# Kernel optimization log

Hardware: AMD Instinct MI355X
Metric: run time of the kernel (lower is better)

## Reference

```python
import jax, jax.numpy as jnp
import numpy as np

N_NODES = 50000


def _sage_conv(x, src, dst, Wl, Wr, b):
    """SAGEConv with mean aggregation: lin_l(mean_j x_j) + lin_r(x_i) + b."""
    msgs = x[src]                                                # [E, Din] gather
    agg = jax.ops.segment_sum(msgs, dst, num_segments=N_NODES)  # [N, Din] scatter-add
    cnt = jax.ops.segment_sum(jnp.ones((src.shape[0], 1), x.dtype), dst,
                              num_segments=N_NODES)             # [N, 1]
    agg = agg / jnp.maximum(cnt, 1.0)                           # mean
    return agg @ Wl.T + x @ Wr.T + b                            # [N, Dout]


def setup_inputs() -> dict:
    key = jax.random.key(0)
    ks = jax.random.split(key, 8)
    d_in, d_h = 64, 128
    x = jax.random.normal(ks[0], (N_NODES, d_in), dtype=jnp.float32)
    edge_index = jax.random.randint(ks[1], (2, 800000), 0, N_NODES, dtype=jnp.int32)
    s1 = 1.0 / np.sqrt(d_in)
    s2 = 1.0 / np.sqrt(d_h)
    return {
        "x": x,
        "edge_index": edge_index,
        "Wl1": jax.random.normal(ks[2], (d_h, d_in), dtype=jnp.float32) * s1,
        "Wr1": jax.random.normal(ks[3], (d_h, d_in), dtype=jnp.float32) * s1,
        "b1": jnp.zeros((d_h,), dtype=jnp.float32),
        "Wl2": jax.random.normal(ks[4], (d_h, d_h), dtype=jnp.float32) * s2,
        "Wr2": jax.random.normal(ks[5], (d_h, d_h), dtype=jnp.float32) * s2,
        "b2": jnp.zeros((d_h,), dtype=jnp.float32),
    }


def reference(x, edge_index, Wl1, Wr1, b1, Wl2, Wr2, b2):
    src, dst = edge_index[0], edge_index[1]
    # layer 1: conv -> dropout(eval: identity) -> ReLU
    h = jax.nn.relu(_sage_conv(x, src, dst, Wl1, Wr1, b1))
    # layer 2
    h = jax.nn.relu(_sage_conv(h, src, dst, Wl2, Wr2, b2))
    return h
```

## Files before the change

kernel.cpp:

```cpp
#include <hip/hip_runtime.h>

#define N_NODES 50000
#define NBUCK 782
#define BCAP 2048
#define BSHIFT 11

typedef __attribute__((ext_vector_type(8))) short short8;
typedef __attribute__((ext_vector_type(4))) float floatx4;
typedef __attribute__((ext_vector_type(2))) float floatx2;
typedef __attribute__((ext_vector_type(2))) int intx2;

static __device__ __forceinline__ unsigned short f2bf(float f) {
  unsigned int u = __builtin_bit_cast(unsigned int, f);
  u += 0x7fff + ((u >> 16) & 1);
  return (unsigned short)(u >> 16);
}
static __device__ __forceinline__ float bf2f(unsigned short s) {
  unsigned int u = ((unsigned int)s) << 16;
  return __builtin_bit_cast(float, u);
}
static __device__ __forceinline__ void fp8x8_acc(intx2 v, floatx2* ac) {
  ac[0] += __builtin_amdgcn_cvt_pk_f32_fp8(v[0], false);
  ac[1] += __builtin_amdgcn_cvt_pk_f32_fp8(v[0], true);
  ac[2] += __builtin_amdgcn_cvt_pk_f32_fp8(v[1], false);
  ac[3] += __builtin_amdgcn_cvt_pk_f32_fp8(v[1], true);
}


__global__ void __launch_bounds__(512) prep_scatter(
    const float* __restrict__ x,
    const float* __restrict__ Wl1, const float* __restrict__ Wr1,
    const float* __restrict__ Wl2, const float* __restrict__ Wr2,
    unsigned short* __restrict__ xb, unsigned char* __restrict__ xq,
    unsigned short* __restrict__ W1, unsigned short* __restrict__ W2,
    const int* __restrict__ src, const int* __restrict__ dst,
    int* __restrict__ bucket_cur, int* __restrict__ buf, int E, int n) {
  const int t = threadIdx.x;
  const int gid = blockIdx.x * 512 + t;
  const int gsz = gridDim.x * 512;
  for (int i = gid; i < n * 16; i += gsz) {
    float4 v = ((const float4*)x)[i];
    unsigned int lo = (unsigned int)f2bf(v.x) | ((unsigned int)f2bf(v.y) << 16);
    unsigned int hi = (unsigned int)f2bf(v.z) | ((unsigned int)f2bf(v.w) << 16);
    ((uint2*)xb)[i] = make_uint2(lo, hi);
    int q = __builtin_amdgcn_cvt_pk_fp8_f32(v.x, v.y, 0, false);
    q = __builtin_amdgcn_cvt_pk_fp8_f32(v.z, v.w, q, true);
    ((int*)xq)[i] = q;
  }
  for (int i = gid; i < 128 * 128; i += gsz) {
    int c = i >> 7, k = i & 127;
    W1[i] = f2bf(k < 64 ? Wl1[c * 64 + k] : Wr1[c * 64 + k - 64]);
  }
  for (int i = gid; i < 128 * 256; i += gsz) {
    int c = i >> 8, k = i & 255;
    W2[i] = f2bf(k < 128 ? Wl2[c * 128 + k] : Wr2[c * 128 + k - 128]);
  }

  __shared__ int hist[NBUCK];
  __shared__ int base_s[NBUCK];
  for (int i = t; i < NBUCK; i += 512) hist[i] = 0;
  __syncthreads();
  int e0 = blockIdx.x * 2048;
  int sv[4], dv[4], bv[4];
#pragma unroll
  for (int p = 0; p < 4; ++p) {
    int e = e0 + p * 512 + t;
    if (e < E) {
      sv[p] = src[e];
      dv[p] = dst[e];
      bv[p] = dv[p] >> 6;
      atomicAdd(&hist[bv[p]], 1);
    } else bv[p] = -1;
  }
  __syncthreads();
  for (int i = t; i < NBUCK; i += 512) {
    int c = hist[i];
    base_s[i] = c > 0 ? atomicAdd(&bucket_cur[i], c) : 0;
  }
  __syncthreads();
  for (int i = t; i < NBUCK; i += 512) hist[i] = 0;
  __syncthreads();
#pragma unroll
  for (int p = 0; p < 4; ++p) {
    if (bv[p] >= 0) {
      int sub = base_s[bv[p]] + atomicAdd(&hist[bv[p]], 1);
      if (sub < BCAP) buf[(bv[p] << BSHIFT) + sub] = (sv[p] << 6) | (dv[p] & 63);
    }
  }
}


__global__ void __launch_bounds__(512, 6) csr_agg_gemm1(
    int* __restrict__ buf, const int* __restrict__ bucket_cur,
    int* __restrict__ row_start, int* __restrict__ row_cnt,
    const unsigned short* __restrict__ xb, const unsigned char* __restrict__ xq,
    const unsigned short* __restrict__ W1, const float* __restrict__ b1,
    unsigned short* __restrict__ h1, unsigned char* __restrict__ h1q, int n) {
  __shared__ int eb[BCAP];
  __shared__ int gsrc[BCAP];
  __shared__ __align__(16) unsigned short aggS[64 * 72];
  __shared__ int cnt[64];
  __shared__ int tmp[64];
  __shared__ int cur[64];
  const int t = threadIdx.x;
  const int b = blockIdx.x;
  const int node0 = b << 6;
  const int len = min(bucket_cur[b], BCAP);
  int* reg = buf + (b << BSHIFT);

  if (t < 64) cnt[t] = 0;
  __syncthreads();
  for (int i = t; i < len; i += 512) {
    int p = reg[i];
    eb[i] = p;
    atomicAdd(&cnt[p & 63], 1);
  }
  __syncthreads();
  if (t < 64) tmp[t] = cnt[t];
  __syncthreads();
#pragma unroll
  for (int off = 1; off < 64; off <<= 1) {
    int u = (t >= off && t < 64) ? tmp[t - off] : 0;
    __syncthreads();
    if (t < 64) tmp[t] += u;
    __syncthreads();
  }
  if (t < 64) {
    int ex = tmp[t] - cnt[t];
    cur[t] = ex;
    int nd = node0 + t;
    if (nd < n) {
      row_start[nd] = (b << BSHIFT) + ex;
      row_cnt[nd] = cnt[t];
    }
  }
  __syncthreads();
  for (int i = t; i < len; i += 512) {
    int p = eb[i];
    int sub = atomicAdd(&cur[p & 63], 1);
    int s = p >> 6;
    gsrc[sub] = s;
    reg[sub] = s;
  }
  __syncthreads();

  const int lane = t & 63;
  const int wv = t >> 6;
  const int eq = lane >> 3;
  const int cl = lane & 7;
  for (int loc = wv; loc < 64; loc += 8) {
    int nd = node0 + loc;
    int cn = (nd < n) ? cnt[loc] : 0;
    int base = tmp[loc] - cnt[loc];
    floatx2 ac[4], ac2[4];
#pragma unroll
    for (int j = 0; j < 4; ++j) { ac[j] = (floatx2){0.f, 0.f}; ac2[j] = (floatx2){0.f, 0.f}; }
    int e = 0;
    for (; e + 16 <= cn; e += 16) {
      int s0 = gsrc[base + e + eq];
      int s1 = gsrc[base + e + 8 + eq];
      intx2 v0 = *(const intx2*)(xq + (size_t)s0 * 64 + cl * 8);
      intx2 v1 = *(const intx2*)(xq + (size_t)s1 * 64 + cl * 8);
      fp8x8_acc(v0, ac);
      fp8x8_acc(v1, ac2);
    }
    for (; e < cn; e += 8) {
      if (e + eq < cn) {
        int s = gsrc[base + e + eq];
        intx2 v = *(const intx2*)(xq + (size_t)s * 64 + cl * 8);
        fp8x8_acc(v, ac);
      }
    }
    float r[8];
#pragma unroll
    for (int j = 0; j < 4; ++j) {
      floatx2 s2 = ac[j] + ac2[j];
      r[2 * j] = s2[0];
      r[2 * j + 1] = s2[1];
    }
#pragma unroll
    for (int j = 0; j < 8; ++j) {
      r[j] += __shfl_xor(r[j], 8, 64);
      r[j] += __shfl_xor(r[j], 16, 64);
      r[j] += __shfl_xor(r[j], 32, 64);
    }
    if (eq == 0) {
      float inv = 1.0f / (float)max(cn, 1);
      short8 o;
#pragma unroll
      for (int j = 0; j < 8; ++j) o[j] = (short)f2bf(r[j] * inv);
      *(short8*)(aggS + loc * 72 + cl * 8) = o;
    }
  }
  __syncthreads();

  const int m = lane & 15;
  const int q = lane >> 4;
  const int rw = (wv & 1) * 32;
  const int cw = (wv >> 1) * 32;
  floatx4 acc[2][2];
#pragma unroll
  for (int rt = 0; rt < 2; ++rt)
#pragma unroll
    for (int ct = 0; ct < 2; ++ct) acc[rt][ct] = (floatx4){0.f, 0.f, 0.f, 0.f};

  int ra = node0 + rw + m;      if (ra > n - 1) ra = n - 1;
  int rb = node0 + rw + 16 + m; if (rb > n - 1) rb = n - 1;
  const unsigned short* selfA0 = xb + (size_t)ra * 64 + q * 8;
  const unsigned short* selfA1 = xb + (size_t)rb * 64 + q * 8;
  const unsigned short* aggL0 = aggS + (rw + m) * 72 + q * 8;
  const unsigned short* aggL1 = aggS + (rw + 16 + m) * 72 + q * 8;
  const unsigned short* Wc0 = W1 + (size_t)(cw + m) * 128 + q * 8;
  const unsigned short* Wc1 = W1 + (size_t)(cw + 16 + m) * 128 + q * 8;

#pragma unroll
  for (int kc = 0; kc < 2; ++kc) {
    short8 a0 = *(const short8*)(aggL0 + kc * 32);
    short8 a1 = *(const short8*)(aggL1 + kc * 32);
    short8 w0 = *(const short8*)(Wc0 + kc * 32);
    short8 w1 = *(const short8*)(Wc1 + kc * 32);
    acc[0][0] = __builtin_amdgcn_mfma_f32_16x16x32_bf16(a0, w0, acc[0][0], 0, 0, 0);
    acc[0][1] = __builtin_amdgcn_mfma_f32_16x16x32_bf16(a0, w1, acc[0][1], 0, 0, 0);
    acc[1][0] = __builtin_amdgcn_mfma_f32_16x16x32_bf16(a1, w0, acc[1][0], 0, 0, 0);
    acc[1][1] = __builtin_amdgcn_mfma_f32_16x16x32_bf16(a1, w1, acc[1][1], 0, 0, 0);
  }
#pragma unroll
  for (int kc = 0; kc < 2; ++kc) {
    short8 a0 = *(const short8*)(selfA0 + kc * 32);
    short8 a1 = *(const short8*)(selfA1 + kc * 32);
    short8 w0 = *(const short8*)(Wc0 + 64 + kc * 32);
    short8 w1 = *(const short8*)(Wc1 + 64 + kc * 32);
    acc[0][0] = __builtin_amdgcn_mfma_f32_16x16x32_bf16(a0, w0, acc[0][0], 0, 0, 0);
    acc[0][1] = __builtin_amdgcn_mfma_f32_16x16x32_bf16(a0, w1, acc[0][1], 0, 0, 0);
    acc[1][0] = __builtin_amdgcn_mfma_f32_16x16x32_bf16(a1, w0, acc[1][0], 0, 0, 0);
    acc[1][1] = __builtin_amdgcn_mfma_f32_16x16x32_bf16(a1, w1, acc[1][1], 0, 0, 0);
  }

  float bv0 = b1[cw + m], bv1 = b1[cw + 16 + m];
#pragma unroll
  for (int rt = 0; rt < 2; ++rt) {
#pragma unroll
    for (int j = 0; j < 4; ++j) {
      int row = node0 + rw + rt * 16 + q * 4 + j;
      if (row < n) {
        float v0 = acc[rt][0][j] + bv0; v0 = v0 > 0.f ? v0 : 0.f;
        float v1 = acc[rt][1][j] + bv1; v1 = v1 > 0.f ? v1 : 0.f;
        h1[(size_t)row * 128 + cw + m] = f2bf(v0);
        h1[(size_t)row * 128 + cw + 16 + m] = f2bf(v1);
        h1q[(size_t)row * 128 + cw + m] =
            (unsigned char)__builtin_amdgcn_cvt_pk_fp8_f32(v0, v0, 0, false);
        h1q[(size_t)row * 128 + cw + 16 + m] =
            (unsigned char)__builtin_amdgcn_cvt_pk_fp8_f32(v1, v1, 0, false);
      }
    }
  }
}


__global__ void __launch_bounds__(512, 6) agg_gemm2(
    const unsigned short* __restrict__ h1, const unsigned char* __restrict__ h1q,
    const int* __restrict__ row_start, const int* __restrict__ row_cnt,
    const int* __restrict__ buf, const unsigned short* __restrict__ W2,
    const float* __restrict__ b2, float* __restrict__ out, int n) {
  __shared__ int gsrcS[BCAP];
  __shared__ __align__(16) unsigned short aggS[64 * 136];
  const int t = threadIdx.x;
  const int lane = t & 63;
  const int wv = t >> 6;
  const int node0 = blockIdx.x << 6;

  {
    const int4* b4 = (const int4*)(buf + ((size_t)blockIdx.x << BSHIFT));
    ((int4*)gsrcS)[t] = b4[t];
  }
  __syncthreads();

  const int eq = lane >> 4;
  const int cl = lane & 15;
#pragma unroll 1
  for (int lp = 0; lp < 4; ++lp) {
    int locA = wv + lp * 16;
    int locB = locA + 8;
    int ndA = node0 + locA, ndB = node0 + locB;
    int cnA = 0, stA = 0, cnB = 0, stB = 0;
    if (ndA < n) { cnA = row_cnt[ndA]; stA = row_start[ndA] - (blockIdx.x << BSHIFT); }
    if (ndB < n) { cnB = row_cnt[ndB]; stB = row_start[ndB] - (blockIdx.x << BSHIFT); }
    floatx2 aA[4], aA2[4], aB[4], aB2[4];
#pragma unroll
    for (int j = 0; j < 4; ++j) {
      aA[j] = (floatx2){0.f, 0.f}; aA2[j] = (floatx2){0.f, 0.f};
      aB[j] = (floatx2){0.f, 0.f}; aB2[j] = (floatx2){0.f, 0.f};
    }
    int mx = max(cnA, cnB);
    for (int e = 0; e < mx; e += 8) {
      if (e + eq < cnA) {
        int s = gsrcS[stA + e + eq];
        intx2 v = *(const intx2*)(h1q + (size_t)s * 128 + cl * 8);
        fp8x8_acc(v, aA);
      }
      if (e + 4 + eq < cnA) {
        int s = gsrcS[stA + e + 4 + eq];
        intx2 v = *(const intx2*)(h1q + (size_t)s * 128 + cl * 8);
        fp8x8_acc(v, aA2);
      }
      if (e + eq < cnB) {
        int s = gsrcS[stB + e + eq];
        intx2 v = *(const intx2*)(h1q + (size_t)s * 128 + cl * 8);
        fp8x8_acc(v, aB);
      }
      if (e + 4 + eq < cnB) {
        int s = gsrcS[stB + e + 4 + eq];
        intx2 v = *(const intx2*)(h1q + (size_t)s * 128 + cl * 8);
        fp8x8_acc(v, aB2);
      }
    }
    float rA[8], rB[8];
#pragma unroll
    for (int j = 0; j < 4; ++j) {
      floatx2 sA = aA[j] + aA2[j];
      rA[2 * j] = sA[0]; rA[2 * j + 1] = sA[1];
      floatx2 sB = aB[j] + aB2[j];
      rB[2 * j] = sB[0]; rB[2 * j + 1] = sB[1];
    }
#pragma unroll
    for (int j = 0; j < 8; ++j) {
      rA[j] += __shfl_xor(rA[j], 16, 64);
      rA[j] += __shfl_xor(rA[j], 32, 64);
      rB[j] += __shfl_xor(rB[j], 16, 64);
      rB[j] += __shfl_xor(rB[j], 32, 64);
    }
    if (eq == 0) {
      float invA = 1.0f / (float)max(cnA, 1);
      float invB = 1.0f / (float)max(cnB, 1);
      short8 oA, oB;
#pragma unroll
      for (int j = 0; j < 8; ++j) { oA[j] = (short)f2bf(rA[j] * invA); oB[j] = (short)f2bf(rB[j] * invB); }
      *(short8*)(aggS + locA * 136 + cl * 8) = oA;
      *(short8*)(aggS + locB * 136 + cl * 8) = oB;
    }
  }
  __syncthreads();

  const int m = lane & 15;
  const int q = lane >> 4;
  const int rw = (wv & 1) * 32;
  const int cw = (wv >> 1) * 32;
  floatx4 acc[2][2];
#pragma unroll
  for (int rt = 0; rt < 2; ++rt)
#pragma unroll
    for (int ct = 0; ct < 2; ++ct) acc[rt][ct] = (floatx4){0.f, 0.f, 0.f, 0.f};

  int ra = node0 + rw + m;      if (ra > n - 1) ra = n - 1;
  int rb = node0 + rw + 16 + m; if (rb > n - 1) rb = n - 1;
  const unsigned short* selfA0 = h1 + (size_t)ra * 128 + q * 8;
  const unsigned short* selfA1 = h1 + (size_t)rb * 128 + q * 8;
  const unsigned short* aggL0 = aggS + (rw + m) * 136 + q * 8;
  const unsigned short* aggL1 = aggS + (rw + 16 + m) * 136 + q * 8;
  const unsigned short* Wc0 = W2 + (size_t)(cw + m) * 256 + q * 8;
  const unsigned short* Wc1 = W2 + (size_t)(cw + 16 + m) * 256 + q * 8;

#pragma unroll
  for (int kc = 0; kc < 4; ++kc) {
    short8 a0 = *(const short8*)(aggL0 + kc * 32);
    short8 a1 = *(const short8*)(aggL1 + kc * 32);
    short8 w0 = *(const short8*)(Wc0 + kc * 32);
    short8 w1 = *(const short8*)(Wc1 + kc * 32);
    acc[0][0] = __builtin_amdgcn_mfma_f32_16x16x32_bf16(a0, w0, acc[0][0], 0, 0, 0);
    acc[0][1] = __builtin_amdgcn_mfma_f32_16x16x32_bf16(a0, w1, acc[0][1], 0, 0, 0);
    acc[1][0] = __builtin_amdgcn_mfma_f32_16x16x32_bf16(a1, w0, acc[1][0], 0, 0, 0);
    acc[1][1] = __builtin_amdgcn_mfma_f32_16x16x32_bf16(a1, w1, acc[1][1], 0, 0, 0);
  }
#pragma unroll
  for (int kc = 0; kc < 4; ++kc) {
    short8 a0 = *(const short8*)(selfA0 + kc * 32);
    short8 a1 = *(const short8*)(selfA1 + kc * 32);
    short8 w0 = *(const short8*)(Wc0 + 128 + kc * 32);
    short8 w1 = *(const short8*)(Wc1 + 128 + kc * 32);
    acc[0][0] = __builtin_amdgcn_mfma_f32_16x16x32_bf16(a0, w0, acc[0][0], 0, 0, 0);
    acc[0][1] = __builtin_amdgcn_mfma_f32_16x16x32_bf16(a0, w1, acc[0][1], 0, 0, 0);
    acc[1][0] = __builtin_amdgcn_mfma_f32_16x16x32_bf16(a1, w0, acc[1][0], 0, 0, 0);
    acc[1][1] = __builtin_amdgcn_mfma_f32_16x16x32_bf16(a1, w1, acc[1][1], 0, 0, 0);
  }

  float bv0 = b2[cw + m], bv1 = b2[cw + 16 + m];
#pragma unroll
  for (int rt = 0; rt < 2; ++rt) {
#pragma unroll
    for (int j = 0; j < 4; ++j) {
      int row = node0 + rw + rt * 16 + q * 4 + j;
      if (row < n) {
        float v0 = acc[rt][0][j] + bv0; v0 = v0 > 0.f ? v0 : 0.f;
        float v1 = acc[rt][1][j] + bv1; v1 = v1 > 0.f ? v1 : 0.f;
        out[(size_t)row * 128 + cw + m] = v0;
        out[(size_t)row * 128 + cw + 16 + m] = v1;
      }
    }
  }
}


extern "C" void kernel_launch(void* const* d_in, const int* in_sizes, int n_in,
                              void* d_out, int out_size, void* d_ws, size_t ws_size,
                              hipStream_t stream) {
  const int N = N_NODES;
  const int E = in_sizes[1] / 2;
  const float* x   = (const float*)d_in[0];
  const int*   src = (const int*)d_in[1];
  const int*   dst = src + E;
  const float* Wl1 = (const float*)d_in[2];
  const float* Wr1 = (const float*)d_in[3];
  const float* b1  = (const float*)d_in[4];
  const float* Wl2 = (const float*)d_in[5];
  const float* Wr2 = (const float*)d_in[6];
  const float* b2  = (const float*)d_in[7];
  float* out = (float*)d_out;

  unsigned short* xb = (unsigned short*)d_ws;
  unsigned short* h1 = xb + (size_t)N * 64;
  unsigned short* W1 = h1 + (size_t)N * 128;
  unsigned short* W2 = W1 + 128 * 128;
  int* row_start  = (int*)(W2 + 128 * 256);
  int* row_cnt    = row_start + N;
  int* bucket_cur = row_cnt + N;
  int* buf        = bucket_cur + 784;
  unsigned char* xq  = (unsigned char*)(buf + (size_t)NBUCK * BCAP);
  unsigned char* h1q = xq + (size_t)N * 64;

  hipMemsetAsync(bucket_cur, 0, NBUCK * sizeof(int), stream);
  int sb = (E + 2047) / 2048;
  prep_scatter<<<sb, 512, 0, stream>>>(x, Wl1, Wr1, Wl2, Wr2, xb, xq, W1, W2,
                                       src, dst, bucket_cur, buf, E, N);
  csr_agg_gemm1<<<NBUCK, 512, 0, stream>>>(buf, bucket_cur, row_start, row_cnt,
                                           xb, xq, W1, b1, h1, h1q, N);
  agg_gemm2<<<NBUCK, 512, 0, stream>>>(h1, h1q, row_start, row_cnt, buf, W2, b2, out, N);
}
```

Measured before the change: 190.0 us.

## Pad CSR rows to multiples of 8 with zero sentinel node and software-pipeline gathers

```diff
diff --git a/kernel.cpp b/kernel.cpp
--- a/kernel.cpp
+++ b/kernel.cpp
@@ -14,10 +14,6 @@
   unsigned int u = __builtin_bit_cast(unsigned int, f);
   u += 0x7fff + ((u >> 16) & 1);
   return (unsigned short)(u >> 16);
-}
-static __device__ __forceinline__ float bf2f(unsigned short s) {
-  unsigned int u = ((unsigned int)s) << 16;
-  return __builtin_bit_cast(float, u);
 }
 static __device__ __forceinline__ void fp8x8_acc(intx2 v, floatx2* ac) {
   ac[0] += __builtin_amdgcn_cvt_pk_f32_fp8(v[0], false);
@@ -47,6 +43,11 @@
     q = __builtin_amdgcn_cvt_pk_fp8_f32(v.z, v.w, q, true);
     ((int*)xq)[i] = q;
   }
+  {
+    unsigned char* h1q = xq + ((size_t)n + 1) * 64;
+    if (gid < 16) ((int*)(xq + (size_t)n * 64))[gid] = 0;
+    if (gid >= 16 && gid < 48) ((int*)(h1q + (size_t)n * 128))[gid - 16] = 0;
+  }
   for (int i = gid; i < 128 * 128; i += gsz) {
     int c = i >> 7, k = i & 127;
     W1[i] = f2bf(k < 64 ? Wl1[c * 64 + k] : Wr1[c * 64 + k - 64]);
@@ -60,10 +61,10 @@
   __shared__ int base_s[NBUCK];
   for (int i = t; i < NBUCK; i += 512) hist[i] = 0;
   __syncthreads();
-  int e0 = blockIdx.x * 2048;
-  int sv[4], dv[4], bv[4];
-#pragma unroll
-  for (int p = 0; p < 4; ++p) {
+  int e0 = blockIdx.x * 4096;
+  int sv[8], dv[8], bv[8];
+#pragma unroll
+  for (int p = 0; p < 8; ++p) {
     int e = e0 + p * 512 + t;
     if (e < E) {
       sv[p] = src[e];
@@ -81,7 +82,7 @@
   for (int i = t; i < NBUCK; i += 512) hist[i] = 0;
   __syncthreads();
 #pragma unroll
-  for (int p = 0; p < 4; ++p) {
+  for (int p = 0; p < 8; ++p) {
     if (bv[p] >= 0) {
       int sub = base_s[bv[p]] + atomicAdd(&hist[bv[p]], 1);
       if (sub < BCAP) buf[(bv[p] << BSHIFT) + sub] = (sv[p] << 6) | (dv[p] & 63);
@@ -116,7 +117,7 @@
     atomicAdd(&cnt[p & 63], 1);
   }
   __syncthreads();
-  if (t < 64) tmp[t] = cnt[t];
+  if (t < 64) tmp[t] = (cnt[t] + 7) & ~7;
   __syncthreads();
 #pragma unroll
   for (int off = 1; off < 64; off <<= 1) {
@@ -126,7 +127,8 @@
     __syncthreads();
   }
   if (t < 64) {
-    int ex = tmp[t] - cnt[t];
+    int c8 = (cnt[t] + 7) & ~7;
+    int ex = tmp[t] - c8;
     cur[t] = ex;
     int nd = node0 + t;
     if (nd < n) {
@@ -139,8 +141,14 @@
     int p = eb[i];
     int sub = atomicAdd(&cur[p & 63], 1);
     int s = p >> 6;
-    gsrc[sub] = s;
-    reg[sub] = s;
+    if (sub < BCAP) { gsrc[sub] = s; reg[sub] = s; }
+  }
+  __syncthreads();
+  if (t < 64) {
+    int c8 = (cnt[t] + 7) & ~7;
+    int e1 = tmp[t];
+    for (int j = e1 - c8 + cnt[t]; j < e1; ++j)
+      if (j < BCAP) { gsrc[j] = n; reg[j] = n; }
   }
   __syncthreads();
 
@@ -148,48 +156,56 @@
   const int wv = t >> 6;
   const int eq = lane >> 3;
   const int cl = lane & 7;
-  for (int loc = wv; loc < 64; loc += 8) {
-    int nd = node0 + loc;
-    int cn = (nd < n) ? cnt[loc] : 0;
-    int base = tmp[loc] - cnt[loc];
-    floatx2 ac[4], ac2[4];
-#pragma unroll
-    for (int j = 0; j < 4; ++j) { ac[j] = (floatx2){0.f, 0.f}; ac2[j] = (floatx2){0.f, 0.f}; }
-    int e = 0;
-    for (; e + 16 <= cn; e += 16) {
-      int s0 = gsrc[base + e + eq];
-      int s1 = gsrc[base + e + 8 + eq];
-      intx2 v0 = *(const intx2*)(xq + (size_t)s0 * 64 + cl * 8);
-      intx2 v1 = *(const intx2*)(xq + (size_t)s1 * 64 + cl * 8);
-      fp8x8_acc(v0, ac);
-      fp8x8_acc(v1, ac2);
-    }
-    for (; e < cn; e += 8) {
-      if (e + eq < cn) {
-        int s = gsrc[base + e + eq];
-        intx2 v = *(const intx2*)(xq + (size_t)s * 64 + cl * 8);
-        fp8x8_acc(v, ac);
-      }
-    }
-    float r[8];
+#pragma unroll 1
+  for (int p = 0; p < 4; ++p) {
+    int locA = wv + p * 16;
+    int locB = locA + 8;
+    int cnA = cnt[locA], cnB = cnt[locB];
+    int cpA = (cnA + 7) & ~7, cpB = (cnB + 7) & ~7;
+    int baseA = tmp[locA] - cpA;
+    int baseB = tmp[locB] - cpB;
+    floatx2 aA[4], aB[4];
+#pragma unroll
+    for (int j = 0; j < 4; ++j) { aA[j] = (floatx2){0.f, 0.f}; aB[j] = (floatx2){0.f, 0.f}; }
+    int mx = max(cpA, cpB);
+    int sA = (0 < cpA) ? gsrc[baseA + eq] : n;
+    int sB = (0 < cpB) ? gsrc[baseB + eq] : n;
+    intx2 vA = *(const intx2*)(xq + (size_t)sA * 64 + cl * 8);
+    intx2 vB = *(const intx2*)(xq + (size_t)sB * 64 + cl * 8);
+    for (int e = 8; e < mx; e += 8) {
+      int sA1 = (e < cpA) ? gsrc[baseA + e + eq] : n;
+      int sB1 = (e < cpB) ? gsrc[baseB + e + eq] : n;
+      intx2 vA1 = *(const intx2*)(xq + (size_t)sA1 * 64 + cl * 8);
+      intx2 vB1 = *(const intx2*)(xq + (size_t)sB1 * 64 + cl * 8);
+      fp8x8_acc(vA, aA);
+      fp8x8_acc(vB, aB);
+      vA = vA1; vB = vB1;
+    }
+    fp8x8_acc(vA, aA);
+    fp8x8_acc(vB, aB);
+    float rA[8], rB[8];
 #pragma unroll
     for (int j = 0; j < 4; ++j) {
-      floatx2 s2 = ac[j] + ac2[j];
-      r[2 * j] = s2[0];
-      r[2 * j + 1] = s2[1];
+      rA[2 * j] = aA[j][0]; rA[2 * j + 1] = aA[j][1];
+      rB[2 * j] = aB[j][0]; rB[2 * j + 1] = aB[j][1];
     }
 #pragma unroll
     for (int j = 0; j < 8; ++j) {
-      r[j] += __shfl_xor(r[j], 8, 64);
-      r[j] += __shfl_xor(r[j], 16, 64);
-      r[j] += __shfl_xor(r[j], 32, 64);
+      rA[j] += __shfl_xor(rA[j], 8, 64);
+      rA[j] += __shfl_xor(rA[j], 16, 64);
+      rA[j] += __shfl_xor(rA[j], 32, 64);
+      rB[j] += __shfl_xor(rB[j], 8, 64);
+      rB[j] += __shfl_xor(rB[j], 16, 64);
+      rB[j] += __shfl_xor(rB[j], 32, 64);
     }
     if (eq == 0) {
-      float inv = 1.0f / (float)max(cn, 1);
-      short8 o;
-#pragma unroll
-      for (int j = 0; j < 8; ++j) o[j] = (short)f2bf(r[j] * inv);
-      *(short8*)(aggS + loc * 72 + cl * 8) = o;
+      float invA = 1.0f / (float)max(cnA, 1);
+      float invB = 1.0f / (float)max(cnB, 1);
+      short8 oA, oB;
+#pragma unroll
+      for (int j = 0; j < 8; ++j) { oA[j] = (short)f2bf(rA[j] * invA); oB[j] = (short)f2bf(rB[j] * invB); }
+      *(short8*)(aggS + locA * 72 + cl * 8) = oA;
+      *(short8*)(aggS + locB * 72 + cl * 8) = oB;
     }
   }
   __syncthreads();
@@ -285,42 +301,40 @@
     int cnA = 0, stA = 0, cnB = 0, stB = 0;
     if (ndA < n) { cnA = row_cnt[ndA]; stA = row_start[ndA] - (blockIdx.x << BSHIFT); }
     if (ndB < n) { cnB = row_cnt[ndB]; stB = row_start[ndB] - (blockIdx.x << BSHIFT); }
-    floatx2 aA[4], aA2[4], aB[4], aB2[4];
+    int cpA = (cnA + 7) & ~7, cpB = (cnB + 7) & ~7;
+    int mx = max(cpA, cpB);
+    floatx2 aA[4], aB[4];
+#pragma unroll
+    for (int j = 0; j < 4; ++j) { aA[j] = (floatx2){0.f, 0.f}; aB[j] = (floatx2){0.f, 0.f}; }
+    int sA0 = (0 < cpA) ? gsrcS[stA + eq] : n;
+    int sA1 = (0 < cpA) ? gsrcS[stA + 4 + eq] : n;
+    int sB0 = (0 < cpB) ? gsrcS[stB + eq] : n;
+    int sB1 = (0 < cpB) ? gsrcS[stB + 4 + eq] : n;
+    intx2 vA0 = *(const intx2*)(h1q + (size_t)sA0 * 128 + cl * 8);
+    intx2 vA1 = *(const intx2*)(h1q + (size_t)sA1 * 128 + cl * 8);
+    intx2 vB0 = *(const intx2*)(h1q + (size_t)sB0 * 128 + cl * 8);
+    intx2 vB1 = *(const intx2*)(h1q + (size_t)sB1 * 128 + cl * 8);
+    for (int e = 8; e < mx; e += 8) {
+      int tA0 = (e < cpA) ? gsrcS[stA + e + eq] : n;
+      int tA1 = (e < cpA) ? gsrcS[stA + e + 4 + eq] : n;
+      int tB0 = (e < cpB) ? gsrcS[stB + e + eq] : n;
+      int tB1 = (e < cpB) ? gsrcS[stB + e + 4 + eq] : n;
+      intx2 wA0 = *(const intx2*)(h1q + (size_t)tA0 * 128 + cl * 8);
+      intx2 wA1 = *(const intx2*)(h1q + (size_t)tA1 * 128 + cl * 8);
+      intx2 wB0 = *(const intx2*)(h1q + (size_t)tB0 * 128 + cl * 8);
+      intx2 wB1 = *(const intx2*)(h1q + (size_t)tB1 * 128 + cl * 8);
+      fp8x8_acc(vA0, aA); fp8x8_acc(vA1, aA);
+      fp8x8_acc(vB0, aB); fp8x8_acc(vB1, aB);
+      vA0 = wA0; vA1 = wA1; vB0 = wB0; vB1 = wB1;
+    }
+    fp8x8_acc(vA0, aA); fp8x8_acc(vA1, aA);
+    fp8x8_acc(vB0, aB); fp8x8_acc(vB1, aB);
+
+    float rA[8], rB[8];
 #pragma unroll
     for (int j = 0; j < 4; ++j) {
-      aA[j] = (floatx2){0.f, 0.f}; aA2[j] = (floatx2){0.f, 0.f};
-      aB[j] = (floatx2){0.f, 0.f}; aB2[j] = (floatx2){0.f, 0.f};
-    }
-    int mx = max(cnA, cnB);
-    for (int e = 0; e < mx; e += 8) {
-      if (e + eq < cnA) {
-        int s = gsrcS[stA + e + eq];
-        intx2 v = *(const intx2*)(h1q + (size_t)s * 128 + cl * 8);
-        fp8x8_acc(v, aA);
-      }
-      if (e + 4 + eq < cnA) {
-        int s = gsrcS[stA + e + 4 + eq];
-        intx2 v = *(const intx2*)(h1q + (size_t)s * 128 + cl * 8);
-        fp8x8_acc(v, aA2);
-      }
-      if (e + eq < cnB) {
-        int s = gsrcS[stB + e + eq];
-        intx2 v = *(const intx2*)(h1q + (size_t)s * 128 + cl * 8);
-        fp8x8_acc(v, aB);
-      }
-      if (e + 4 + eq < cnB) {
-        int s = gsrcS[stB + e + 4 + eq];
-        intx2 v = *(const intx2*)(h1q + (size_t)s * 128 + cl * 8);
-        fp8x8_acc(v, aB2);
-      }
-    }
-    float rA[8], rB[8];
-#pragma unroll
-    for (int j = 0; j < 4; ++j) {
-      floatx2 sA = aA[j] + aA2[j];
-      rA[2 * j] = sA[0]; rA[2 * j + 1] = sA[1];
-      floatx2 sB = aB[j] + aB2[j];
-      rB[2 * j] = sB[0]; rB[2 * j + 1] = sB[1];
+      rA[2 * j] = aA[j][0]; rA[2 * j + 1] = aA[j][1];
+      rB[2 * j] = aB[j][0]; rB[2 * j + 1] = aB[j][1];
     }
 #pragma unroll
     for (int j = 0; j < 8; ++j) {
@@ -425,10 +439,10 @@
   int* bucket_cur = row_cnt + N;
   int* buf        = bucket_cur + 784;
   unsigned char* xq  = (unsigned char*)(buf + (size_t)NBUCK * BCAP);
-  unsigned char* h1q = xq + (size_t)N * 64;
-
-  hipMemsetAsync(bucket_cur, 0, NBUCK * sizeof(int), stream);
-  int sb = (E + 2047) / 2048;
+  unsigned char* h1q = xq + ((size_t)N + 1) * 64;
+
+  (void)hipMemsetAsync(bucket_cur, 0, NBUCK * sizeof(int), stream);
+  int sb = (E + 4095) / 4096;
   prep_scatter<<<sb, 512, 0, stream>>>(x, Wl1, Wr1, Wl2, Wr2, xb, xq, W1, W2,
                                        src, dst, bucket_cur, buf, E, N);
   csr_agg_gemm1<<<NBUCK, 512, 0, stream>>>(buf, bucket_cur, row_start, row_cnt,
```

Measured after the change: 185.1 us. -2.6%, faster.
